# Kernel optimization log

Hardware: AMD Instinct MI355X
Metric: run time of the kernel (lower is better)

## Reference

```python
import jax, jax.numpy as jnp
import numpy as np

B, S, H = 64, 4096, 256

def setup_inputs() -> dict:
    key = jax.random.key(0)
    k1, k2, k3, k4, k5 = jax.random.split(key, 5)
    scale = 1.0 / np.sqrt(H)
    return {
        "enc_out": jax.random.normal(k1, (B, S, H), dtype=jnp.float32),
        "final_h": jax.random.normal(k2, (B, H), dtype=jnp.float32),
        "W1": jax.random.normal(k3, (H, H), dtype=jnp.float32) * scale,
        "W2": jax.random.normal(k4, (H, H), dtype=jnp.float32) * scale,
        "v": jax.random.normal(k5, (H,), dtype=jnp.float32) * scale,
    }

def reference(enc_out, final_h, W1, W2, v):
    # W1(enc_out): [B,S,H]; W2(final_h) computed once: [B,H], broadcast over S
    proj = jnp.einsum('bsh,kh->bsk', enc_out, W1) + jnp.einsum('bh,kh->bk', final_h, W2)[:, None, :]
    scores = jnp.einsum('bsk,k->bs', jnp.tanh(proj), v)  # [B,S]
    alpha = jax.nn.softmax(scores, axis=1)  # softmax over seq dim
    context = jnp.einsum('bs,bsh->bh', alpha, enc_out)  # [B,H]
    return context
```

## Files before the change

kernel.cpp:

```cpp
#include <hip/hip_runtime.h>

typedef _Float16 half8  __attribute__((ext_vector_type(8)));
typedef _Float16 half4_t __attribute__((ext_vector_type(4)));
typedef float    f32x4  __attribute__((ext_vector_type(4)));

#define B_SZ    64
#define S_SZ    4096
#define H_SZ    256
#define CHUNKS  8
#define SCHUNK  512
#define TILE_R  64
#define NTILES  (SCHUNK / TILE_R)
#define PAD_H   264

__device__ __forceinline__ float tanh_fast(float x) {
  return 1.f - 2.f * __builtin_amdgcn_rcpf(__expf(2.f * x) + 1.f);
}

__device__ __forceinline__ void lds_barrier() {
  asm volatile("s_waitcnt lgkmcnt(0)" ::: "memory");
  __builtin_amdgcn_s_barrier();
}

template<int CTRL>
__device__ __forceinline__ float dpp_add_shl(float x) {
  int s = __builtin_amdgcn_update_dpp(0, __builtin_bit_cast(int, x), CTRL, 0xf, 0xf, true);
  return x + __builtin_bit_cast(float, s);
}
__device__ __forceinline__ float row_reduce16(float x) {
  x = dpp_add_shl<0x108>(x);
  x = dpp_add_shl<0x104>(x);
  x = dpp_add_shl<0x102>(x);
  x = dpp_add_shl<0x101>(x);
  return x;
}

__global__ __launch_bounds__(256) void bias_kernel(const float* __restrict__ fh,
                                                   const float* __restrict__ W2,
                                                   float* __restrict__ bias) {
  const int b = blockIdx.x, k = threadIdx.x;
  __shared__ float fsh[H_SZ];
  fsh[k] = fh[b * H_SZ + k];
  __syncthreads();
  const float* wrow = W2 + (size_t)k * H_SZ;
  float s = 0.f;
#pragma unroll 4
  for (int h = 0; h < H_SZ; h += 4) {
    f32x4 w = *(const f32x4*)(wrow + h);
    s += w[0] * fsh[h] + w[1] * fsh[h + 1] + w[2] * fsh[h + 2] + w[3] * fsh[h + 3];
  }
  bias[b * H_SZ + k] = s;
}

__global__ __launch_bounds__(512, 2) void fused_kernel(const float* __restrict__ enc,
                                                       const float* __restrict__ W1,
                                                       const float* __restrict__ v,
                                                       const float* __restrict__ bias,
                                                       float* __restrict__ pc,
                                                       float* __restrict__ pl) {
  __shared__ _Float16 As[2][TILE_R][PAD_H] __attribute__((aligned(16)));
  __shared__ float spartT[TILE_R][12];
  __shared__ float cpart[8][H_SZ];
  __shared__ float lArr[8];

  const int tid  = threadIdx.x;
  const int wave = tid >> 6;
  const int lane = tid & 63;
  const int nlo  = lane & 15;
  const int g    = lane >> 4;
  const int khi  = g * 8;
  const int b     = blockIdx.x >> 3;
  const int chunk = blockIdx.x & 7;
  const size_t encBase = ((size_t)b * S_SZ + (size_t)chunk * SCHUNK) * H_SZ;

  f32x4 ld[8];
  {
    const float* src = enc + encBase + (size_t)tid * 4;
#pragma unroll
    for (int i = 0; i < 8; ++i) ld[i] = *(const f32x4*)(src + i * 2048);
  }

  half8 wf[2][8];
#pragma unroll
  for (int cf = 0; cf < 2; ++cf) {
    const int n = wave * 32 + cf * 16 + nlo;
    const float* wrow = W1 + (size_t)n * H_SZ + khi;
#pragma unroll
    for (int ks = 0; ks < 8; ++ks) {
      f32x4 w0 = *(const f32x4*)(wrow + ks * 32);
      f32x4 w1 = *(const f32x4*)(wrow + ks * 32 + 4);
      half8 h;
#pragma unroll
      for (int j = 0; j < 4; ++j) { h[j] = (_Float16)w0[j]; h[4 + j] = (_Float16)w1[j]; }
      wf[cf][ks] = h;
    }
  }
  const int n0c = wave * 32 + nlo;
  const float vv0 = v[n0c],               vv1 = v[n0c + 16];
  const float bv0 = bias[b * H_SZ + n0c], bv1 = bias[b * H_SZ + n0c + 16];

  float l_acc = 0.f;
  float c0 = 0.f, c1 = 0.f, c2 = 0.f, c3 = 0.f;

#pragma unroll 1
  for (int t = 0; t < NTILES; ++t) {
    const int p = t & 1;
    const bool pf = (t < NTILES - 1);
    const float* srcN = enc + encBase + (size_t)(t + 1) * TILE_R * H_SZ + (size_t)tid * 4;

#pragma unroll
    for (int i = 0; i < 4; ++i) {
      const int f4 = tid + i * 512;
      const int r = f4 >> 6, hq = (f4 & 63) * 4;
      half4_t hv;
      hv[0] = (_Float16)ld[i][0]; hv[1] = (_Float16)ld[i][1];
      hv[2] = (_Float16)ld[i][2]; hv[3] = (_Float16)ld[i][3];
      *(half4_t*)&As[p][r][hq] = hv;
    }
    if (pf) {
#pragma unroll
      for (int i = 0; i < 4; ++i) ld[i] = *(const f32x4*)(srcN + i * 2048);
    }
#pragma unroll
    for (int i = 4; i < 8; ++i) {
      const int f4 = tid + i * 512;
      const int r = f4 >> 6, hq = (f4 & 63) * 4;
      half4_t hv;
      hv[0] = (_Float16)ld[i][0]; hv[1] = (_Float16)ld[i][1];
      hv[2] = (_Float16)ld[i][2]; hv[3] = (_Float16)ld[i][3];
      *(half4_t*)&As[p][r][hq] = hv;
    }
    if (pf) {
#pragma unroll
      for (int i = 4; i < 8; ++i) ld[i] = *(const f32x4*)(srcN + i * 2048);
    }
    lds_barrier();

#pragma unroll
    for (int rf = 0; rf < 4; ++rf) {
      f32x4 d0 = {bv0, bv0, bv0, bv0}, d1 = {bv1, bv1, bv1, bv1};
#pragma unroll
      for (int ks = 0; ks < 8; ++ks) {
        half8 a = *(const half8*)&As[p][rf * 16 + nlo][ks * 32 + khi];
        d0 = __builtin_amdgcn_mfma_f32_16x16x32_f16(a, wf[0][ks], d0, 0, 0, 0);
        d1 = __builtin_amdgcn_mfma_f32_16x16x32_f16(a, wf[1][ks], d1, 0, 0, 0);
      }
      f32x4 s4;
#pragma unroll
      for (int i = 0; i < 4; ++i)
        s4[i] = tanh_fast(d0[i]) * vv0 + tanh_fast(d1[i]) * vv1;
#pragma unroll
      for (int i = 0; i < 4; ++i) s4[i] = row_reduce16(s4[i]);
      if (nlo == 0) {
#pragma unroll
        for (int i = 0; i < 4; ++i) spartT[rf * 16 + g * 4 + i][wave] = s4[i];
      }
    }
    lds_barrier();

#pragma unroll
    for (int rr = 0; rr < 8; ++rr) {
      const int r = wave * 8 + rr;
      const f32x4 q0 = *(const f32x4*)&spartT[r][0];
      const f32x4 q1 = *(const f32x4*)&spartT[r][4];
      const float u = __expf(q0[0] + q0[1] + q0[2] + q0[3] + q1[0] + q1[1] + q1[2] + q1[3]);
      l_acc += u;
      half4_t a = *(const half4_t*)&As[p][r][lane * 4];
      c0 += u * (float)a[0];
      c1 += u * (float)a[1];
      c2 += u * (float)a[2];
      c3 += u * (float)a[3];
    }
  }

  {
    f32x4 cv; cv[0] = c0; cv[1] = c1; cv[2] = c2; cv[3] = c3;
    *(f32x4*)&cpart[wave][lane * 4] = cv;
  }
  if (lane == 0) lArr[wave] = l_acc;
  __syncthreads();
  if (tid < H_SZ) {
    float s = 0.f;
#pragma unroll
    for (int w = 0; w < 8; ++w) s += cpart[w][tid];
    pc[(size_t)blockIdx.x * H_SZ + tid] = s;
  }
  if (tid == 0) {
    float L = 0.f;
#pragma unroll
    for (int w = 0; w < 8; ++w) L += lArr[w];
    pl[blockIdx.x] = L;
  }
}

__global__ __launch_bounds__(256) void combine_kernel(const float* __restrict__ pc,
                                                      const float* __restrict__ pl,
                                                      float* __restrict__ out) {
  const int b = blockIdx.x, h = threadIdx.x;
  float L = 0.f, s = 0.f;
#pragma unroll
  for (int j = 0; j < CHUNKS; ++j) {
    L += pl[b * CHUNKS + j];
    s += pc[(size_t)(b * CHUNKS + j) * H_SZ + h];
  }
  out[b * H_SZ + h] = s / L;
}

extern "C" void kernel_launch(void* const* d_in, const int* in_sizes, int n_in,
                              void* d_out, int out_size, void* d_ws, size_t ws_size,
                              hipStream_t stream) {
  const float* enc = (const float*)d_in[0];
  const float* fh  = (const float*)d_in[1];
  const float* W1  = (const float*)d_in[2];
  const float* W2  = (const float*)d_in[3];
  const float* v   = (const float*)d_in[4];
  float* out = (float*)d_out;

  float* ws   = (float*)d_ws;
  float* bias = ws;
  float* pc   = ws + B_SZ * H_SZ;
  float* pl   = pc + B_SZ * CHUNKS * H_SZ;

  bias_kernel<<<B_SZ, H_SZ, 0, stream>>>(fh, W2, bias);
  fused_kernel<<<B_SZ * CHUNKS, 512, 0, stream>>>(enc, W1, v, bias, pc, pl);
  combine_kernel<<<B_SZ, H_SZ, 0, stream>>>(pc, pl, out);
}
```

Measured before the change: 90.65 us.

## Halve tile rows and software-pipeline softmax-context stage with triple-buffered LDS

```diff
diff --git a/kernel.cpp b/kernel.cpp
--- a/kernel.cpp
+++ b/kernel.cpp
@@ -9,7 +9,7 @@
 #define H_SZ    256
 #define CHUNKS  8
 #define SCHUNK  512
-#define TILE_R  64
+#define TILE_R  32
 #define NTILES  (SCHUNK / TILE_R)
 #define PAD_H   264
 
@@ -58,8 +58,8 @@
                                                        const float* __restrict__ bias,
                                                        float* __restrict__ pc,
                                                        float* __restrict__ pl) {
-  __shared__ _Float16 As[2][TILE_R][PAD_H] __attribute__((aligned(16)));
-  __shared__ float spartT[TILE_R][12];
+  __shared__ _Float16 As[3][TILE_R][PAD_H] __attribute__((aligned(16)));
+  __shared__ float spartT[2][TILE_R][12];
   __shared__ float cpart[8][H_SZ];
   __shared__ float lArr[8];
 
@@ -73,11 +73,11 @@
   const int chunk = blockIdx.x & 7;
   const size_t encBase = ((size_t)b * S_SZ + (size_t)chunk * SCHUNK) * H_SZ;
 
-  f32x4 ld[8];
+  f32x4 ld[4];
   {
     const float* src = enc + encBase + (size_t)tid * 4;
 #pragma unroll
-    for (int i = 0; i < 8; ++i) ld[i] = *(const f32x4*)(src + i * 2048);
+    for (int i = 0; i < 4; ++i) ld[i] = *(const f32x4*)(src + i * 2048);
   }
 
   half8 wf[2][8];
@@ -102,9 +102,11 @@
   float l_acc = 0.f;
   float c0 = 0.f, c1 = 0.f, c2 = 0.f, c3 = 0.f;
 
+  int p = 0;
+  int pm1 = 2;
+
 #pragma unroll 1
   for (int t = 0; t < NTILES; ++t) {
-    const int p = t & 1;
     const bool pf = (t < NTILES - 1);
     const float* srcN = enc + encBase + (size_t)(t + 1) * TILE_R * H_SZ + (size_t)tid * 4;
 
@@ -121,23 +123,10 @@
 #pragma unroll
       for (int i = 0; i < 4; ++i) ld[i] = *(const f32x4*)(srcN + i * 2048);
     }
-#pragma unroll
-    for (int i = 4; i < 8; ++i) {
-      const int f4 = tid + i * 512;
-      const int r = f4 >> 6, hq = (f4 & 63) * 4;
-      half4_t hv;
-      hv[0] = (_Float16)ld[i][0]; hv[1] = (_Float16)ld[i][1];
-      hv[2] = (_Float16)ld[i][2]; hv[3] = (_Float16)ld[i][3];
-      *(half4_t*)&As[p][r][hq] = hv;
-    }
-    if (pf) {
-#pragma unroll
-      for (int i = 4; i < 8; ++i) ld[i] = *(const f32x4*)(srcN + i * 2048);
-    }
     lds_barrier();
 
 #pragma unroll
-    for (int rf = 0; rf < 4; ++rf) {
+    for (int rf = 0; rf < 2; ++rf) {
       f32x4 d0 = {bv0, bv0, bv0, bv0}, d1 = {bv1, bv1, bv1, bv1};
 #pragma unroll
       for (int ks = 0; ks < 8; ++ks) {
@@ -153,19 +142,40 @@
       for (int i = 0; i < 4; ++i) s4[i] = row_reduce16(s4[i]);
       if (nlo == 0) {
 #pragma unroll
-        for (int i = 0; i < 4; ++i) spartT[rf * 16 + g * 4 + i][wave] = s4[i];
+        for (int i = 0; i < 4; ++i) spartT[t & 1][rf * 16 + g * 4 + i][wave] = s4[i];
       }
     }
-    lds_barrier();
-
-#pragma unroll
-    for (int rr = 0; rr < 8; ++rr) {
-      const int r = wave * 8 + rr;
-      const f32x4 q0 = *(const f32x4*)&spartT[r][0];
-      const f32x4 q1 = *(const f32x4*)&spartT[r][4];
+
+    if (t > 0) {
+#pragma unroll
+      for (int rr = 0; rr < 4; ++rr) {
+        const int r = wave * 4 + rr;
+        const f32x4 q0 = *(const f32x4*)&spartT[(t - 1) & 1][r][0];
+        const f32x4 q1 = *(const f32x4*)&spartT[(t - 1) & 1][r][4];
+        const float u = __expf(q0[0] + q0[1] + q0[2] + q0[3] + q1[0] + q1[1] + q1[2] + q1[3]);
+        l_acc += u;
+        half4_t a = *(const half4_t*)&As[pm1][r][lane * 4];
+        c0 += u * (float)a[0];
+        c1 += u * (float)a[1];
+        c2 += u * (float)a[2];
+        c3 += u * (float)a[3];
+      }
+    }
+    pm1 = p;
+    p = (p == 2) ? 0 : p + 1;
+  }
+
+  lds_barrier();
+  {
+    const int tl = (NTILES - 1) & 1;
+#pragma unroll
+    for (int rr = 0; rr < 4; ++rr) {
+      const int r = wave * 4 + rr;
+      const f32x4 q0 = *(const f32x4*)&spartT[tl][r][0];
+      const f32x4 q1 = *(const f32x4*)&spartT[tl][r][4];
       const float u = __expf(q0[0] + q0[1] + q0[2] + q0[3] + q1[0] + q1[1] + q1[2] + q1[3]);
       l_acc += u;
-      half4_t a = *(const half4_t*)&As[p][r][lane * 4];
+      half4_t a = *(const half4_t*)&As[pm1][r][lane * 4];
       c0 += u * (float)a[0];
       c1 += u * (float)a[1];
       c2 += u * (float)a[2];
```

Measured after the change: 87.97 us. 1.03x faster.

## Stream encoder tiles into LDS via direct global-to-LDS DMA with XOR swizzle

Applied to the files above, without the earlier changes.

```diff
diff --git a/kernel.cpp b/kernel.cpp
--- a/kernel.cpp
+++ b/kernel.cpp
@@ -1,17 +1,16 @@
 #include <hip/hip_runtime.h>
 
 typedef _Float16 half8  __attribute__((ext_vector_type(8)));
-typedef _Float16 half4_t __attribute__((ext_vector_type(4)));
 typedef float    f32x4  __attribute__((ext_vector_type(4)));
+typedef unsigned int uint4_t __attribute__((ext_vector_type(4)));
 
 #define B_SZ    64
 #define S_SZ    4096
 #define H_SZ    256
 #define CHUNKS  8
 #define SCHUNK  512
-#define TILE_R  64
+#define TILE_R  32
 #define NTILES  (SCHUNK / TILE_R)
-#define PAD_H   264
 
 __device__ __forceinline__ float tanh_fast(float x) {
   return 1.f - 2.f * __builtin_amdgcn_rcpf(__expf(2.f * x) + 1.f);
@@ -20,6 +19,13 @@
 __device__ __forceinline__ void lds_barrier() {
   asm volatile("s_waitcnt lgkmcnt(0)" ::: "memory");
   __builtin_amdgcn_s_barrier();
+}
+
+__device__ __forceinline__ void gll16(const float* g, float* l) {
+  __builtin_amdgcn_global_load_lds(
+      (const __attribute__((address_space(1))) unsigned int*)g,
+      (__attribute__((address_space(3))) unsigned int*)l,
+      16, 0, 0);
 }
 
 template<int CTRL>
@@ -58,9 +64,8 @@
                                                        const float* __restrict__ bias,
                                                        float* __restrict__ pc,
                                                        float* __restrict__ pl) {
-  __shared__ _Float16 As[2][TILE_R][PAD_H] __attribute__((aligned(16)));
+  __shared__ float As[2][TILE_R][H_SZ] __attribute__((aligned(16)));
   __shared__ float spartT[TILE_R][12];
-  __shared__ float cpart[8][H_SZ];
   __shared__ float lArr[8];
 
   const int tid  = threadIdx.x;
@@ -69,16 +74,22 @@
   const int nlo  = lane & 15;
   const int g    = lane >> 4;
   const int khi  = g * 8;
+  const int x7   = lane & 7;
   const int b     = blockIdx.x >> 3;
   const int chunk = blockIdx.x & 7;
   const size_t encBase = ((size_t)b * S_SZ + (size_t)chunk * SCHUNK) * H_SZ;
-
-  f32x4 ld[8];
-  {
-    const float* src = enc + encBase + (size_t)tid * 4;
-#pragma unroll
-    for (int i = 0; i < 8; ++i) ld[i] = *(const f32x4*)(src + i * 2048);
-  }
+  const int srcg = (lane ^ wave) << 2;
+
+  auto issue_dma = [&](int t, int buf) {
+    const float* gt = enc + encBase + (size_t)t * TILE_R * H_SZ;
+#pragma unroll
+    for (int i = 0; i < 4; ++i) {
+      const int row = i * 8 + wave;
+      gll16(gt + (size_t)row * H_SZ + srcg, &As[buf][row][0]);
+    }
+  };
+
+  issue_dma(0, 0);
 
   half8 wf[2][8];
 #pragma unroll
@@ -99,49 +110,45 @@
   const float vv0 = v[n0c],               vv1 = v[n0c + 16];
   const float bv0 = bias[b * H_SZ + n0c], bv1 = bias[b * H_SZ + n0c + 16];
 
+  issue_dma(1, 1);
+
+  int offA[8], offB[8];
+  {
+    const int hb = g * 2;
+#pragma unroll
+    for (int ks = 0; ks < 8; ++ks) {
+      const int g0 = ks * 8 + hb;
+      offA[ks] = ((g0 ^ x7) << 4);
+      offB[ks] = (((g0 + 1) ^ x7) << 4);
+    }
+  }
+  const int rb0 = nlo * 1024;
+  const int rb1 = rb0 + 16384;
+
   float l_acc = 0.f;
   float c0 = 0.f, c1 = 0.f, c2 = 0.f, c3 = 0.f;
 
-#pragma unroll 1
-  for (int t = 0; t < NTILES; ++t) {
-    const int p = t & 1;
-    const bool pf = (t < NTILES - 1);
-    const float* srcN = enc + encBase + (size_t)(t + 1) * TILE_R * H_SZ + (size_t)tid * 4;
-
-#pragma unroll
-    for (int i = 0; i < 4; ++i) {
-      const int f4 = tid + i * 512;
-      const int r = f4 >> 6, hq = (f4 & 63) * 4;
-      half4_t hv;
-      hv[0] = (_Float16)ld[i][0]; hv[1] = (_Float16)ld[i][1];
-      hv[2] = (_Float16)ld[i][2]; hv[3] = (_Float16)ld[i][3];
-      *(half4_t*)&As[p][r][hq] = hv;
-    }
-    if (pf) {
-#pragma unroll
-      for (int i = 0; i < 4; ++i) ld[i] = *(const f32x4*)(srcN + i * 2048);
-    }
-#pragma unroll
-    for (int i = 4; i < 8; ++i) {
-      const int f4 = tid + i * 512;
-      const int r = f4 >> 6, hq = (f4 & 63) * 4;
-      half4_t hv;
-      hv[0] = (_Float16)ld[i][0]; hv[1] = (_Float16)ld[i][1];
-      hv[2] = (_Float16)ld[i][2]; hv[3] = (_Float16)ld[i][3];
-      *(half4_t*)&As[p][r][hq] = hv;
-    }
-    if (pf) {
-#pragma unroll
-      for (int i = 4; i < 8; ++i) ld[i] = *(const f32x4*)(srcN + i * 2048);
-    }
-    lds_barrier();
-
-#pragma unroll
-    for (int rf = 0; rf < 4; ++rf) {
+  auto tile_body = [&](int t, bool last) {
+    if (last) asm volatile("s_waitcnt vmcnt(0)" ::: "memory");
+    else      asm volatile("s_waitcnt vmcnt(4)" ::: "memory");
+    __builtin_amdgcn_s_barrier();
+
+    const char* asb = (const char*)&As[t & 1][0][0];
+
+#pragma unroll
+    for (int rf = 0; rf < 2; ++rf) {
+      const int rb = rf ? rb1 : rb0;
       f32x4 d0 = {bv0, bv0, bv0, bv0}, d1 = {bv1, bv1, bv1, bv1};
 #pragma unroll
       for (int ks = 0; ks < 8; ++ks) {
-        half8 a = *(const half8*)&As[p][rf * 16 + nlo][ks * 32 + khi];
+        const f32x4 a0 = *(const f32x4*)(asb + rb + offA[ks]);
+        const f32x4 a1 = *(const f32x4*)(asb + rb + offB[ks]);
+        uint4_t u;
+        u[0] = __builtin_bit_cast(unsigned int, __builtin_amdgcn_cvt_pkrtz(a0[0], a0[1]));
+        u[1] = __builtin_bit_cast(unsigned int, __builtin_amdgcn_cvt_pkrtz(a0[2], a0[3]));
+        u[2] = __builtin_bit_cast(unsigned int, __builtin_amdgcn_cvt_pkrtz(a1[0], a1[1]));
+        u[3] = __builtin_bit_cast(unsigned int, __builtin_amdgcn_cvt_pkrtz(a1[2], a1[3]));
+        const half8 a = __builtin_bit_cast(half8, u);
         d0 = __builtin_amdgcn_mfma_f32_16x16x32_f16(a, wf[0][ks], d0, 0, 0, 0);
         d1 = __builtin_amdgcn_mfma_f32_16x16x32_f16(a, wf[1][ks], d1, 0, 0, 0);
       }
@@ -159,30 +166,39 @@
     lds_barrier();
 
 #pragma unroll
-    for (int rr = 0; rr < 8; ++rr) {
-      const int r = wave * 8 + rr;
+    for (int rr = 0; rr < 4; ++rr) {
+      const int r = wave * 4 + rr;
       const f32x4 q0 = *(const f32x4*)&spartT[r][0];
       const f32x4 q1 = *(const f32x4*)&spartT[r][4];
       const float u = __expf(q0[0] + q0[1] + q0[2] + q0[3] + q1[0] + q1[1] + q1[2] + q1[3]);
       l_acc += u;
-      half4_t a = *(const half4_t*)&As[p][r][lane * 4];
-      c0 += u * (float)a[0];
-      c1 += u * (float)a[1];
-      c2 += u * (float)a[2];
-      c3 += u * (float)a[3];
-    }
-  }
-
+      const f32x4 av = *(const f32x4*)(asb + r * 1024 + ((lane ^ (r & 7)) << 4));
+      c0 += u * av[0];
+      c1 += u * av[1];
+      c2 += u * av[2];
+      c3 += u * av[3];
+    }
+    lds_barrier();
+
+    if (t + 2 < NTILES) issue_dma(t + 2, t & 1);
+  };
+
+#pragma unroll 1
+  for (int t = 0; t < NTILES - 1; ++t) tile_body(t, false);
+  tile_body(NTILES - 1, true);
+
+  float* cpart = (float*)&As[0][0][0];
+  float* crow  = cpart + wave * H_SZ;
   {
     f32x4 cv; cv[0] = c0; cv[1] = c1; cv[2] = c2; cv[3] = c3;
-    *(f32x4*)&cpart[wave][lane * 4] = cv;
+    *(f32x4*)(crow + lane * 4) = cv;
   }
   if (lane == 0) lArr[wave] = l_acc;
   __syncthreads();
   if (tid < H_SZ) {
     float s = 0.f;
 #pragma unroll
-    for (int w = 0; w < 8; ++w) s += cpart[w][tid];
+    for (int w = 0; w < 8; ++w) s += cpart[w * H_SZ + tid];
     pc[(size_t)blockIdx.x * H_SZ + tid] = s;
   }
   if (tid == 0) {
```

Result: slower. 103.0 us (+13.7%).
